# Kernel tuning notes

Hardware: AMD Instinct MI355X
Metric: run time of the kernel (lower is better)

## Reference

```python
import jax, jax.numpy as jnp
import numpy as np

H = 5  # hidden size of both LSTMs

def _lstm_layer(x, Wih, Whh, bih, bhh):
    """x: [B,T,I] -> hs: [B,T,H]. PyTorch gate order i,f,g,o; zero init state."""
    B, T, _ = x.shape
    # precompute input contribution for all timesteps: [T,B,4H]
    xg = (jnp.einsum('bti,gi->btg', x, Wih) + bih + bhh).transpose(1, 0, 2)
    def step(carry, xg_t):
        h, c = carry
        g = xg_t + h @ Whh.T
        i, f, gg, o = jnp.split(g, 4, axis=-1)
        c = jax.nn.sigmoid(f) * c + jax.nn.sigmoid(i) * jnp.tanh(gg)
        h = jax.nn.sigmoid(o) * jnp.tanh(c)
        return (h, c), h
    h0 = jnp.zeros((B, H), x.dtype)
    (_, _), hs = jax.lax.scan(step, (h0, h0), xg)
    return hs.transpose(1, 0, 2)  # [B,T,H]

def setup_inputs() -> dict:
    key = jax.random.key(0)
    ks = jax.random.split(key, 32)
    B, T = 16384, 128
    def u(k, shape, fan):
        s = 1.0 / np.sqrt(fan)
        return jax.random.uniform(k, shape, jnp.float32, -s, s)
    inp = {
        'x1': jax.random.normal(ks[0], (B, T, 5), jnp.float32),
        'x2': jax.random.normal(ks[1], (B, T, 5), jnp.float32),
        # lstm1 (1 layer)
        'Wih1': u(ks[2], (4*H, 5), H), 'Whh1': u(ks[3], (4*H, H), H),
        'bih1': u(ks[4], (4*H,), H), 'bhh1': u(ks[5], (4*H,), H),
        # lstm2 layer 0
        'Wih2a': u(ks[6], (4*H, 5), H), 'Whh2a': u(ks[7], (4*H, H), H),
        'bih2a': u(ks[8], (4*H,), H), 'bhh2a': u(ks[9], (4*H,), H),
        # lstm2 layer 1
        'Wih2b': u(ks[10], (4*H, H), H), 'Whh2b': u(ks[11], (4*H, H), H),
        'bih2b': u(ks[12], (4*H,), H), 'bhh2b': u(ks[13], (4*H,), H),
        # FC stack 20->32->32->16->16->5
        'W1': u(ks[14], (32, 20), 20), 'b1': u(ks[15], (32,), 20),
        'W2': u(ks[16], (32, 32), 32), 'b2': u(ks[17], (32,), 32),
        'W3': u(ks[18], (16, 32), 32), 'b3': u(ks[19], (16,), 32),
        'W4': u(ks[20], (16, 16), 16), 'b4': u(ks[21], (16,), 16),
        'W5': u(ks[22], (5, 16), 16), 'b5': u(ks[23], (5,), 16),
    }
    return inp

def reference(x1, x2, Wih1, Whh1, bih1, bhh1, Wih2a, Whh2a, bih2a, bhh2a,
              Wih2b, Whh2b, bih2b, bhh2b, W1, b1, W2, b2, W3, b3, W4, b4, W5, b5):
    out1 = _lstm_layer(x1, Wih1, Whh1, bih1, bhh1)[:, -1, :]            # [B,5]
    h2 = _lstm_layer(x2, Wih2a, Whh2a, bih2a, bhh2a)                    # [B,T,5]
    out2 = _lstm_layer(h2, Wih2b, Whh2b, bih2b, bhh2b)[:, -1, :]        # [B,5]
    out = jnp.concatenate([x1[:, -1, :], x2[:, -1, :], out1, out2], axis=1)  # [B,20]
    out = jax.nn.relu(out @ W1.T + b1)
    out = jax.nn.relu(out @ W2.T + b2)
    out = jax.nn.relu(out @ W3.T + b3)
    out = jax.nn.relu(out @ W4.T + b4)
    return out @ W5.T + b5  # [B,5]
```

## Files before the change

### kernel.cpp

```cpp
#include <hip/hip_runtime.h>

#define DEV __device__ __forceinline__
#define KSIG (-1.442695041f)
#define KTANH (-2.885390082f)

typedef float f2 __attribute__((ext_vector_type(2)));

DEV float fexp2(float x) { return __builtin_amdgcn_exp2f(x); }
DEV float frcp(float x) { return __builtin_amdgcn_rcpf(x); }
DEV float bperm(int a, float x) {
  return __int_as_float(__builtin_amdgcn_ds_bpermute(a, __float_as_int(x)));
}
DEV f2 pkfma(f2 a, f2 b, f2 c) { return __builtin_elementwise_fma(a, b, c); }

struct CellP {
  f2 wx[4][2];
  f2 wh[4][2];
  float wx4[4], wh4[4];
  f2 b2[4];
};

DEV void load_cellP(CellP& W, int u, const float* __restrict__ Wih,
                    const float* __restrict__ Whh,
                    const float* __restrict__ bih,
                    const float* __restrict__ bhh) {
#pragma unroll
  for (int rt = 0; rt < 4; ++rt) {
    int row = 5 * rt + u;
    float kx = (rt == 2) ? KTANH : KSIG;
    W.wx[rt][0] = (f2){kx * Wih[row * 5 + 0], kx * Wih[row * 5 + 1]};
    W.wx[rt][1] = (f2){kx * Wih[row * 5 + 2], kx * Wih[row * 5 + 3]};
    W.wx4[rt] = kx * Wih[row * 5 + 4];
    W.wh[rt][0] = (f2){kx * Whh[row * 5 + 0], kx * Whh[row * 5 + 1]};
    W.wh[rt][1] = (f2){kx * Whh[row * 5 + 2], kx * Whh[row * 5 + 3]};
    W.wh4[rt] = kx * Whh[row * 5 + 4];
    W.b2[rt] = (f2){kx * (bih[row] + bhh[row]), 0.f};
  }
}

DEV float stepP(const CellP& W, const f2 xp[2], float x4, float hAll[5],
                float& c, const int bp[5]) {
  f2 hp0 = (f2){hAll[0], hAll[1]};
  f2 hp1 = (f2){hAll[2], hAll[3]};
  float acc[4];
#pragma unroll
  for (int rt = 0; rt < 4; ++rt) {
    f2 a2 = pkfma(W.wh[rt][0], hp0, W.b2[rt]);
    a2 = pkfma(W.wh[rt][1], hp1, a2);
    a2 = pkfma(W.wx[rt][0], xp[0], a2);
    a2 = pkfma(W.wx[rt][1], xp[1], a2);
    float a = a2.x + a2.y;
    a = fmaf(W.wh4[rt], hAll[4], a);
    acc[rt] = fmaf(W.wx4[rt], x4, a);
  }
  float gi = frcp(1.f + fexp2(acc[0]));
  float gf = frcp(1.f + fexp2(acc[1]));
  float gg = fmaf(2.f, frcp(1.f + fexp2(acc[2])), -1.f);
  float go = frcp(1.f + fexp2(acc[3]));
  c = fmaf(gf, c, gi * gg);
  float th = fmaf(2.f, frcp(1.f + fexp2(KTANH * c)), -1.f);
  float h = go * th;
#pragma unroll
  for (int u2 = 0; u2 < 5; ++u2) hAll[u2] = bperm(bp[u2], h);
  return h;
}

__global__ __launch_bounds__(192, 2) void rnn_stag_kernel(
    const float* __restrict__ x1, const float* __restrict__ x2,
    const float* __restrict__ Wih1, const float* __restrict__ Whh1,
    const float* __restrict__ bih1, const float* __restrict__ bhh1,
    const float* __restrict__ Wih2a, const float* __restrict__ Whh2a,
    const float* __restrict__ bih2a, const float* __restrict__ bhh2a,
    const float* __restrict__ Wih2b, const float* __restrict__ Whh2b,
    const float* __restrict__ bih2b, const float* __restrict__ bhh2b,
    const float* __restrict__ W1, const float* __restrict__ b1,
    const float* __restrict__ W2, const float* __restrict__ b2,
    const float* __restrict__ W3, const float* __restrict__ b3,
    const float* __restrict__ W4, const float* __restrict__ b4,
    const float* __restrict__ W5, const float* __restrict__ b5,
    float* __restrict__ out, int B) {
  __shared__ float sIn[24][20];
  __shared__ float sA[24][32];
  __shared__ float sB[24][32];

  const int tid = threadIdx.x;
  const int w = tid >> 6;
  const int l = tid & 63;
  int g = l / 5;
  const int u = l - 5 * g;
  const bool act = (g < 12);
  if (!act) g = 11;
  const int base = blockIdx.x * 24;

  int bp[5];
#pragma unroll
  for (int k = 0; k < 5; ++k) bp[k] = (5 * g + k) * 4;

  if (w == 0) {
    CellP W;
    load_cellP(W, u, Wih1, Whh1, bih1, bhh1);
    const int e0 = base + 2 * g, e1 = e0 + 1;
    const int e0c = (e0 < B) ? e0 : B - 1;
    const int e1c = (e1 < B) ? e1 : B - 1;
    const float* p0 = x1 + (size_t)e0c * 640;
    const float* p1 = x1 + (size_t)e1c * 640;
    float h0[5], h1[5];
    float c0 = 0.f, c1 = 0.f, ho0 = 0.f, ho1 = 0.f;
#pragma unroll
    for (int k = 0; k < 5; ++k) {
      h0[k] = 0.f;
      h1[k] = 0.f;
    }
    f2 xa[2] = {(f2){p0[0], p0[1]}, (f2){p0[2], p0[3]}};
    f2 xb[2] = {(f2){p1[0], p1[1]}, (f2){p1[2], p1[3]}};
    float xa4 = p0[4], xb4 = p1[4];
    for (int t = 0; t < 128; ++t) {
      f2 xia[2] = {xa[0], xa[1]}, xib[2] = {xb[0], xb[1]};
      float xia4 = xa4, xib4 = xb4;
      const int tn = (t < 127) ? t + 1 : 127;
      xa[0] = (f2){p0[tn * 5 + 0], p0[tn * 5 + 1]};
      xa[1] = (f2){p0[tn * 5 + 2], p0[tn * 5 + 3]};
      xa4 = p0[tn * 5 + 4];
      xb[0] = (f2){p1[tn * 5 + 0], p1[tn * 5 + 1]};
      xb[1] = (f2){p1[tn * 5 + 2], p1[tn * 5 + 3]};
      xb4 = p1[tn * 5 + 4];
      ho0 = stepP(W, xia, xia4, h0, c0, bp);
      ho1 = stepP(W, xib, xib4, h1, c1, bp);
    }
    if (act) {
      sIn[2 * g][u] = x1[(size_t)e0c * 640 + 635 + u];
      sIn[2 * g][10 + u] = ho0;
      sIn[2 * g + 1][u] = x1[(size_t)e1c * 640 + 635 + u];
      sIn[2 * g + 1][10 + u] = ho1;
    }
  } else {
    CellP Wa, Wb;
    load_cellP(Wa, u, Wih2a, Whh2a, bih2a, bhh2a);
    load_cellP(Wb, u, Wih2b, Whh2b, bih2b, bhh2b);
    const int el = ((w == 1) ? 0 : 12) + g;
    const int e = base + el;
    const int ec = (e < B) ? e : B - 1;
    const float* px = x2 + (size_t)ec * 640;
    float hA[5], hB[5];
    float cA = 0.f, cB = 0.f, hoB = 0.f;
#pragma unroll
    for (int k = 0; k < 5; ++k) {
      hA[k] = 0.f;
      hB[k] = 0.f;
    }
    f2 xc[2] = {(f2){px[0], px[1]}, (f2){px[2], px[3]}};
    float xc4 = px[4];
    (void)stepP(Wa, xc, xc4, hA, cA, bp);
    xc[0] = (f2){px[5], px[6]};
    xc[1] = (f2){px[7], px[8]};
    xc4 = px[9];
    for (int t = 1; t < 128; ++t) {
      f2 xin[2] = {xc[0], xc[1]};
      float xin4 = xc4;
      const int tn = (t < 127) ? t + 1 : 127;
      xc[0] = (f2){px[tn * 5 + 0], px[tn * 5 + 1]};
      xc[1] = (f2){px[tn * 5 + 2], px[tn * 5 + 3]};
      xc4 = px[tn * 5 + 4];
      f2 hin[2] = {(f2){hA[0], hA[1]}, (f2){hA[2], hA[3]}};
      float hin4 = hA[4];
      (void)stepP(Wa, xin, xin4, hA, cA, bp);
      hoB = stepP(Wb, hin, hin4, hB, cB, bp);
    }
    {
      f2 hin[2] = {(f2){hA[0], hA[1]}, (f2){hA[2], hA[3]}};
      hoB = stepP(Wb, hin, hA[4], hB, cB, bp);
    }
    if (act) {
      sIn[el][5 + u] = x2[(size_t)ec * 640 + 635 + u];
      sIn[el][15 + u] = hoB;
    }
  }
  __syncthreads();

  for (int task = tid; task < 24 * 32; task += 192) {
    int e = task >> 5, n = task & 31;
    float acc = b1[n];
#pragma unroll
    for (int k = 0; k < 20; ++k) acc = fmaf(W1[n * 20 + k], sIn[e][k], acc);
    sA[e][n] = fmaxf(acc, 0.f);
  }
  __syncthreads();
  for (int task = tid; task < 24 * 32; task += 192) {
    int e = task >> 5, n = task & 31;
    float acc = b2[n];
#pragma unroll
    for (int k = 0; k < 32; ++k) acc = fmaf(W2[n * 32 + k], sA[e][k], acc);
    sB[e][n] = fmaxf(acc, 0.f);
  }
  __syncthreads();
  for (int task = tid; task < 24 * 16; task += 192) {
    int e = task >> 4, n = task & 15;
    float acc = b3[n];
#pragma unroll
    for (int k = 0; k < 32; ++k) acc = fmaf(W3[n * 32 + k], sB[e][k], acc);
    sA[e][n] = fmaxf(acc, 0.f);
  }
  __syncthreads();
  for (int task = tid; task < 24 * 16; task += 192) {
    int e = task >> 4, n = task & 15;
    float acc = b4[n];
#pragma unroll
    for (int k = 0; k < 16; ++k) acc = fmaf(W4[n * 16 + k], sA[e][k], acc);
    sB[e][n] = fmaxf(acc, 0.f);
  }
  __syncthreads();
  if (tid < 120) {
    int e = tid / 5, n = tid - 5 * (tid / 5);
    float acc = b5[n];
#pragma unroll
    for (int k = 0; k < 16; ++k) acc = fmaf(W5[n * 16 + k], sB[e][k], acc);
    int ego = base + e;
    if (ego < B) out[(size_t)ego * 5 + n] = acc;
  }
}

extern "C" void kernel_launch(void* const* d_in, const int* in_sizes, int n_in,
                              void* d_out, int out_size, void* d_ws,
                              size_t ws_size, hipStream_t stream) {
  const float* x1 = (const float*)d_in[0];
  const float* x2 = (const float*)d_in[1];
  const float* Wih1 = (const float*)d_in[2];
  const float* Whh1 = (const float*)d_in[3];
  const float* bih1 = (const float*)d_in[4];
  const float* bhh1 = (const float*)d_in[5];
  const float* Wih2a = (const float*)d_in[6];
  const float* Whh2a = (const float*)d_in[7];
  const float* bih2a = (const float*)d_in[8];
  const float* bhh2a = (const float*)d_in[9];
  const float* Wih2b = (const float*)d_in[10];
  const float* Whh2b = (const float*)d_in[11];
  const float* bih2b = (const float*)d_in[12];
  const float* bhh2b = (const float*)d_in[13];
  const float* W1 = (const float*)d_in[14];
  const float* b1 = (const float*)d_in[15];
  const float* W2 = (const float*)d_in[16];
  const float* b2 = (const float*)d_in[17];
  const float* W3 = (const float*)d_in[18];
  const float* b3 = (const float*)d_in[19];
  const float* W4 = (const float*)d_in[20];
  const float* b4 = (const float*)d_in[21];
  const float* W5 = (const float*)d_in[22];
  const float* b5 = (const float*)d_in[23];

  int B = in_sizes[0] / 640;
  int nB = (B + 23) / 24;

  rnn_stag_kernel<<<nB, 192, 0, stream>>>(
      x1, x2, Wih1, Whh1, bih1, bhh1, Wih2a, Whh2a, bih2a, bhh2a, Wih2b, Whh2b,
      bih2b, bhh2b, W1, b1, W2, b2, W3, b3, W4, b4, W5, b5, (float*)d_out, B);
}
```

Baseline: 237.8 us.

## Split fused LSTM kernel into two launches via workspace for layer-2b

Replaces the single staggered kernel with two kernels when a workspace buffer is available. The first runs LSTM1 and LSTM2 layer 0 on separate waves and writes the full layer-0 hidden sequence and LSTM1's last state to global memory. The second runs layer 1 from that buffer and then the FC stack. This exposes more independent recurrences per wave and raises occupancy, at the cost of writing and re-reading about 42 MB of intermediate hidden states and a second launch.

```diff
diff --git a/kernel.cpp b/kernel.cpp
--- a/kernel.cpp
+++ b/kernel.cpp
@@ -5,6 +5,7 @@
 #define KTANH (-2.885390082f)
 
 typedef float f2 __attribute__((ext_vector_type(2)));
+typedef float f4 __attribute__((ext_vector_type(4)));
 
 DEV float fexp2(float x) { return __builtin_amdgcn_exp2f(x); }
 DEV float frcp(float x) { return __builtin_amdgcn_rcpf(x); }
@@ -63,6 +64,200 @@
 #pragma unroll
   for (int u2 = 0; u2 < 5; ++u2) hAll[u2] = bperm(bp[u2], h);
   return h;
+}
+
+struct XBuf {
+  f4 a, b, c, d, e;
+};
+DEV void xload(XBuf& bf, const float* __restrict__ px, int ch) {
+  const f4* q = (const f4*)px + ch * 5;
+  bf.a = q[0];
+  bf.b = q[1];
+  bf.c = q[2];
+  bf.d = q[3];
+  bf.e = q[4];
+}
+
+__global__ __launch_bounds__(192, 3) void rnn_a_kernel(
+    const float* __restrict__ x1, const float* __restrict__ x2,
+    const float* __restrict__ Wih1, const float* __restrict__ Whh1,
+    const float* __restrict__ bih1, const float* __restrict__ bhh1,
+    const float* __restrict__ Wih2a, const float* __restrict__ Whh2a,
+    const float* __restrict__ bih2a, const float* __restrict__ bhh2a,
+    float* __restrict__ h2a, float* __restrict__ h1l, int B, int N1) {
+  const int tid = threadIdx.x;
+  const int wid = blockIdx.x * 3 + (tid >> 6);
+  if (wid >= 2 * N1) return;
+  const int l = tid & 63;
+  int g = l / 5;
+  const int u = l - 5 * g;
+  const bool act = (g < 12);
+  if (!act) g = 11;
+  const bool r2 = (wid >= N1);
+  const int e = (r2 ? wid - N1 : wid) * 12 + g;
+  const int ec = (e < B) ? e : B - 1;
+
+  CellP W;
+  if (r2)
+    load_cellP(W, u, Wih2a, Whh2a, bih2a, bhh2a);
+  else
+    load_cellP(W, u, Wih1, Whh1, bih1, bhh1);
+
+  int bp[5];
+#pragma unroll
+  for (int k = 0; k < 5; ++k) bp[k] = (5 * g + k) * 4;
+
+  const float* px = (r2 ? x2 : x1) + (size_t)ec * 640;
+  const bool wr = r2 && act && (e < B);
+  float* ps = h2a + (size_t)ec * 640 + u;
+
+  float hAll[5];
+  float c = 0.f, hOwn = 0.f;
+#pragma unroll
+  for (int k = 0; k < 5; ++k) hAll[k] = 0.f;
+
+#define SA1(S, xa, xb, xc, xd, xe)                  \
+  {                                                 \
+    f2 xin[2] = {(f2){xa, xb}, (f2){xc, xd}};       \
+    hOwn = stepP(W, xin, xe, hAll, c, bp);          \
+    if (wr) pst[(S) * 5] = hOwn;                    \
+  }
+#define CHUNKA(X)                                  \
+  SA1(0, X.a.x, X.a.y, X.a.z, X.a.w, X.b.x)        \
+  SA1(1, X.b.y, X.b.z, X.b.w, X.c.x, X.c.y)        \
+  SA1(2, X.c.z, X.c.w, X.d.x, X.d.y, X.d.z)        \
+  SA1(3, X.d.w, X.e.x, X.e.y, X.e.z, X.e.w)
+
+  XBuf A0, B0;
+  xload(A0, px, 0);
+  for (int ch = 0; ch < 32; ch += 2) {
+    xload(B0, px, (ch + 1 < 32) ? ch + 1 : 31);
+    {
+      float* pst = ps + (size_t)ch * 20;
+      CHUNKA(A0);
+    }
+    xload(A0, px, (ch + 2 < 32) ? ch + 2 : 31);
+    {
+      float* pst = ps + (size_t)(ch + 1) * 20;
+      CHUNKA(B0);
+    }
+  }
+#undef SA1
+#undef CHUNKA
+
+  if (!r2 && act && e < B) h1l[(size_t)e * 5 + u] = hOwn;
+}
+
+__global__ __launch_bounds__(192, 2) void rnn_b_kernel(
+    const float* __restrict__ x1, const float* __restrict__ x2,
+    const float* __restrict__ Wih2b, const float* __restrict__ Whh2b,
+    const float* __restrict__ bih2b, const float* __restrict__ bhh2b,
+    const float* __restrict__ W1, const float* __restrict__ b1,
+    const float* __restrict__ W2, const float* __restrict__ b2,
+    const float* __restrict__ W3, const float* __restrict__ b3,
+    const float* __restrict__ W4, const float* __restrict__ b4,
+    const float* __restrict__ W5, const float* __restrict__ b5,
+    const float* __restrict__ h2a, const float* __restrict__ h1l,
+    float* __restrict__ out, int B) {
+  __shared__ float sIn[36][20];
+  __shared__ float sA[36][32];
+  __shared__ float sB[36][32];
+
+  const int tid = threadIdx.x;
+  const int w = tid >> 6;
+  const int l = tid & 63;
+  int g = l / 5;
+  const int u = l - 5 * g;
+  const bool act = (g < 12);
+  if (!act) g = 11;
+  const int el = w * 12 + g;
+  const int e = blockIdx.x * 36 + el;
+  const int ec = (e < B) ? e : B - 1;
+
+  CellP W;
+  load_cellP(W, u, Wih2b, Whh2b, bih2b, bhh2b);
+
+  int bp[5];
+#pragma unroll
+  for (int k = 0; k < 5; ++k) bp[k] = (5 * g + k) * 4;
+
+  const float* ph = h2a + (size_t)ec * 640;
+
+  float hAll[5];
+  float c = 0.f, hOwn = 0.f;
+#pragma unroll
+  for (int k = 0; k < 5; ++k) hAll[k] = 0.f;
+
+#define SB1(xa, xb, xc, xd, xe)                 \
+  {                                             \
+    f2 xin[2] = {(f2){xa, xb}, (f2){xc, xd}};   \
+    hOwn = stepP(W, xin, xe, hAll, c, bp);      \
+  }
+#define CHUNKB(X)                              \
+  SB1(X.a.x, X.a.y, X.a.z, X.a.w, X.b.x)       \
+  SB1(X.b.y, X.b.z, X.b.w, X.c.x, X.c.y)       \
+  SB1(X.c.z, X.c.w, X.d.x, X.d.y, X.d.z)       \
+  SB1(X.d.w, X.e.x, X.e.y, X.e.z, X.e.w)
+
+  XBuf A0, B0;
+  xload(A0, ph, 0);
+  for (int ch = 0; ch < 32; ch += 2) {
+    xload(B0, ph, (ch + 1 < 32) ? ch + 1 : 31);
+    CHUNKB(A0);
+    xload(A0, ph, (ch + 2 < 32) ? ch + 2 : 31);
+    CHUNKB(B0);
+  }
+#undef SB1
+#undef CHUNKB
+
+  if (act) {
+    sIn[el][u] = x1[(size_t)ec * 640 + 635 + u];
+    sIn[el][5 + u] = x2[(size_t)ec * 640 + 635 + u];
+    sIn[el][10 + u] = h1l[(size_t)ec * 5 + u];
+    sIn[el][15 + u] = hOwn;
+  }
+  __syncthreads();
+
+  for (int task = tid; task < 36 * 32; task += 192) {
+    int e2 = task >> 5, n = task & 31;
+    float acc = b1[n];
+#pragma unroll
+    for (int k = 0; k < 20; ++k) acc = fmaf(W1[n * 20 + k], sIn[e2][k], acc);
+    sA[e2][n] = fmaxf(acc, 0.f);
+  }
+  __syncthreads();
+  for (int task = tid; task < 36 * 32; task += 192) {
+    int e2 = task >> 5, n = task & 31;
+    float acc = b2[n];
+#pragma unroll
+    for (int k = 0; k < 32; ++k) acc = fmaf(W2[n * 32 + k], sA[e2][k], acc);
+    sB[e2][n] = fmaxf(acc, 0.f);
+  }
+  __syncthreads();
+  for (int task = tid; task < 36 * 16; task += 192) {
+    int e2 = task >> 4, n = task & 15;
+    float acc = b3[n];
+#pragma unroll
+    for (int k = 0; k < 32; ++k) acc = fmaf(W3[n * 32 + k], sB[e2][k], acc);
+    sA[e2][n] = fmaxf(acc, 0.f);
+  }
+  __syncthreads();
+  for (int task = tid; task < 36 * 16; task += 192) {
+    int e2 = task >> 4, n = task & 15;
+    float acc = b4[n];
+#pragma unroll
+    for (int k = 0; k < 16; ++k) acc = fmaf(W4[n * 16 + k], sA[e2][k], acc);
+    sB[e2][n] = fmaxf(acc, 0.f);
+  }
+  __syncthreads();
+  for (int task = tid; task < 36 * 5; task += 192) {
+    int e2 = task / 5, n = task - 5 * (task / 5);
+    float acc = b5[n];
+#pragma unroll
+    for (int k = 0; k < 16; ++k) acc = fmaf(W5[n * 16 + k], sB[e2][k], acc);
+    int ego = blockIdx.x * 36 + e2;
+    if (ego < B) out[(size_t)ego * 5 + n] = acc;
+  }
 }
 
 __global__ __launch_bounds__(192, 2) void rnn_stag_kernel(
@@ -248,9 +443,24 @@
   const float* b5 = (const float*)d_in[23];
 
   int B = in_sizes[0] / 640;
-  int nB = (B + 23) / 24;
-
-  rnn_stag_kernel<<<nB, 192, 0, stream>>>(
-      x1, x2, Wih1, Whh1, bih1, bhh1, Wih2a, Whh2a, bih2a, bhh2a, Wih2b, Whh2b,
-      bih2b, bhh2b, W1, b1, W2, b2, W3, b3, W4, b4, W5, b5, (float*)d_out, B);
-}
+  size_t req = ((size_t)B * 640 + (size_t)B * 5) * sizeof(float);
+
+  if (d_ws && ws_size >= req) {
+    float* h2a = (float*)d_ws;
+    float* h1l = h2a + (size_t)B * 640;
+    int N1 = (B + 11) / 12;
+    int nA = (2 * N1 + 2) / 3;
+    int nB = (B + 35) / 36;
+    rnn_a_kernel<<<nA, 192, 0, stream>>>(x1, x2, Wih1, Whh1, bih1, bhh1, Wih2a,
+                                         Whh2a, bih2a, bhh2a, h2a, h1l, B, N1);
+    rnn_b_kernel<<<nB, 192, 0, stream>>>(x1, x2, Wih2b, Whh2b, bih2b, bhh2b,
+                                         W1, b1, W2, b2, W3, b3, W4, b4, W5,
+                                         b5, h2a, h1l, (float*)d_out, B);
+  } else {
+    int nB = (B + 23) / 24;
+    rnn_stag_kernel<<<nB, 192, 0, stream>>>(
+        x1, x2, Wih1, Whh1, bih1, bhh1, Wih2a, Whh2a, bih2a, bhh2a, Wih2b,
+        Whh2b, bih2b, bhh2b, W1, b1, W2, b2, W3, b3, W4, b4, W5, b5,
+        (float*)d_out, B);
+  }
+}
```

Result: no change. 242.0 us (+1.8%).
